# Optimization experiments

Measured on AMD Instinct MI355X. Metric: run time of the kernel, lower is better.

Reference implementation:

```python
import jax, jax.numpy as jnp
import numpy as np

# Static dims (chosen so check_image_size padding is a no-op)
B, C, H, W = 4, 96, 256, 256
NUM_HEADS = 4
WIN_PARAM = 8          # number of windows per dim
SUB = 4                # sub-window pixel size
WIN_H = H // WIN_PARAM  # 32: window pixel size
WIN_W = W // WIN_PARAM
SCALE = (C // NUM_HEADS) ** -0.5


def setup_inputs() -> dict:
    key = jax.random.key(0)
    ks = jax.random.split(key, 4)
    s = 0.02
    return {
        "x": jax.random.normal(ks[0], (B, C, H, W), jnp.float32),
        "q_w": jax.random.normal(ks[1], (C, C), jnp.float32) * s,
        "q_b": jnp.zeros((C,), jnp.float32),
        "kv_w": jax.random.normal(ks[2], (2 * C, C), jnp.float32) * s,
        "kv_b": jnp.zeros((2 * C,), jnp.float32),
        "proj_w": jax.random.normal(ks[3], (C, C), jnp.float32) * s,
        "proj_b": jnp.zeros((C,), jnp.float32),
    }


def reference(x, q_w, q_b, kv_w, kv_b, proj_w, proj_b):
    nWh, nWw = H // WIN_H, W // WIN_W
    nW = nWh * nWw                      # 64 windows
    swh, sww = WIN_H // SUB, WIN_W // SUB
    sNW = swh * sww                     # 64 sub-windows per window
    N = SUB * SUB                       # 16 tokens per sub-window
    d = C // NUM_HEADS

    # B C (nWh wH) (nWw wW) -> B nW wH wW C
    wx = x.reshape(B, C, nWh, WIN_H, nWw, WIN_W).transpose(0, 2, 4, 3, 5, 1)
    wx = wx.reshape(B, nW, WIN_H, WIN_W, C)
    # B nW (swh sub)(sww sub) C -> B nW sNW N C
    sx = wx.reshape(B, nW, swh, SUB, sww, SUB, C).transpose(0, 1, 2, 4, 3, 5, 6)
    sx = sx.reshape(B, nW, sNW, N, C)
    # shuffle: B sNW nW N C
    sh = sx.transpose(0, 2, 1, 3, 4)
    pooled = sh.mean(axis=3)                     # B sNW nW C
    merged = sh.reshape(B, sNW, nW * N, C)       # B sNW (nW N) C

    q = pooled @ q_w.T + q_b                     # B sNW nW C
    kv = merged @ kv_w.T + kv_b                  # B sNW nW*N 2C
    k, v = kv[..., :C], kv[..., C:]

    q = q.reshape(B, sNW, nW, NUM_HEADS, d).transpose(0, 1, 3, 2, 4) * SCALE
    k = k.reshape(B, sNW, nW * N, NUM_HEADS, d).transpose(0, 1, 3, 2, 4)
    v = v.reshape(B, sNW, nW * N, NUM_HEADS, d).transpose(0, 1, 3, 2, 4)

    attn = jax.nn.softmax(jnp.einsum('bshqd,bshkd->bshqk', q, k), axis=-1)
    o = jnp.einsum('bshqk,bshkd->bshqd', attn, v)          # B sNW nH nW d

    # B sNW nH nW d -> B nW sNW (nH d)
    o = o.transpose(0, 3, 1, 2, 4).reshape(B, nW, sNW, C)
    o = o @ proj_w.T + proj_b

    # broadcast each sub-window result to its N tokens (repeat)
    o = jnp.broadcast_to(o[:, :, :, None, :], (B, nW, sNW, N, C))
    # B nW (swh sww)(sub sub) C -> B nW wH wW C
    o = o.reshape(B, nW, swh, sww, SUB, SUB, C).transpose(0, 1, 2, 4, 3, 5, 6)
    o = o.reshape(B, nW, WIN_H, WIN_W, C)
    # B (nWh nWw) wH wW C -> B C H W
    o = o.reshape(B, nWh, nWw, WIN_H, WIN_W, C).transpose(0, 5, 1, 3, 2, 4)
    return o.reshape(B, C, H, W)
```

## Files before the change

### kernel.cpp

```cpp
#include <hip/hip_runtime.h>
#include <hip/hip_bf16.h>
#include <stdint.h>

#define PLANE 65536
#define SCALE_F 0.20412414523193154f
#define PPART 1572864
#define PSTRIDE_F2 786432
#define TI_STRIDE 1572864

typedef __attribute__((ext_vector_type(8))) short short8;
typedef __attribute__((ext_vector_type(4))) float f32x4;

__device__ __forceinline__ unsigned pk2(float a, float b) {
  union { __hip_bfloat162 h; unsigned u; } cv;
  cv.h = __float22bfloat162_rn(make_float2(a, b));
  return cv.u;
}

__global__ __launch_bounds__(256) void prep_kernel(
    const float* __restrict__ kvw, unsigned short* __restrict__ w_a1,
    unsigned short* __restrict__ w_b2) {
  int tid = blockIdx.x * 256 + threadIdx.x;
  int side = tid / 1536;
  int r = tid % 1536;
  int frag = r >> 6;
  int lane = r & 63;
  int tile = frag / 3, ks = frag % 3;
  int od = tile * 16 + (lane & 15);
  int c0 = ks * 32 + (lane >> 4) * 8;
  int h = od >> 5, dd = od & 31;
  unsigned out[4] = {0u, 0u, 0u, 0u};
  if (dd < 24) {
    int row = (side == 0) ? (h * 24 + dd) : (96 + h * 24 + dd);
    const float* src = kvw + row * 96 + c0;
    float4 f0 = *(const float4*)src;
    float4 f1 = *(const float4*)(src + 4);
    out[0] = pk2(f0.x, f0.y); out[1] = pk2(f0.z, f0.w);
    out[2] = pk2(f1.x, f1.y); out[3] = pk2(f1.z, f1.w);
  }
  unsigned* dst =
      (unsigned*)((side == 0) ? w_a1 : w_b2) + (frag * 64 + lane) * 4;
  dst[0] = out[0]; dst[1] = out[1]; dst[2] = out[2]; dst[3] = out[3];
}

__global__ __launch_bounds__(512) void tp_kernel(const float* __restrict__ x,
                                                 unsigned short* __restrict__ xT,
                                                 float2* __restrict__ part2) {
  __shared__ unsigned Lq[48 * 128];
  int blk = blockIdx.x;
  int h = blk & 1;
  int pr = (blk >> 1) & 3;
  int swr = (blk >> 3) & 7;
  int wh = (blk >> 6) & 7;
  int b = blk >> 9;
  int t = threadIdx.x;
  int c4l = t & 31;
  int cpg = t >> 5;
  int ka = c4l >> 3;

  int r = wh * 32 + swr * 4 + pr;
  const float* xrow =
      x + ((size_t)(b * 96) * 256 + r) * 256 + (h * 32 + c4l) * 4;

  float2 pout[3];
  #pragma unroll
  for (int j = 0; j < 3; ++j) {
    int cpair = j * 16 + cpg;
    int cg = cpair >> 2;
    const float* pA = xrow + (size_t)(2 * cpair) * PLANE;
    float4 vA = *(const float4*)pA;
    float4 vB = *(const float4*)(pA + PLANE);
    pout[j].x = (vA.x + vA.y) + (vA.z + vA.w);
    pout[j].y = (vB.x + vB.y) + (vB.z + vB.w);
    unsigned w0 = pk2(vA.x, vB.x), w1 = pk2(vA.y, vB.y);
    unsigned w2 = pk2(vA.z, vB.z), w3 = pk2(vA.w, vB.w);
    int K = ka | ((cg & 7) << 2);
    int base = cpair * 128;
    int c0 = 4 * c4l;
    Lq[base + ((c0 + 0) ^ K)] = w0;
    Lq[base + ((c0 + 1) ^ K)] = w1;
    Lq[base + ((c0 + 2) ^ K)] = w2;
    Lq[base + ((c0 + 3) ^ K)] = w3;
  }

  {
    float2* pp = part2 +
        ((size_t)(((pr * 4 + b) * 8 + swr) * 8 + wh) * 2 + h) * 1536;
    #pragma unroll
    for (int j = 0; j < 3; ++j) pp[j * 512 + t] = pout[j];
  }
  __syncthreads();

  uint4* dst = (uint4*)xT + (size_t)(b * 256 + r) * 3072;
  #pragma unroll
  for (int it = 0; it < 3; ++it) {
    int id = it * 512 + t;
    int sw = id / 192;
    int r1 = id - sw * 192;
    int cg = r1 >> 4;
    int r2 = r1 & 15;
    int pw = r2 >> 2, wwl = r2 & 3;
    int coll = wwl * 32 + sw * 4 + pw;
    int K = wwl | ((cg & 7) << 2);
    int cx = coll ^ K;
    unsigned q0 = Lq[(cg * 4 + 0) * 128 + cx];
    unsigned q1 = Lq[(cg * 4 + 1) * 128 + cx];
    unsigned q2 = Lq[(cg * 4 + 2) * 128 + cx];
    unsigned q3 = Lq[(cg * 4 + 3) * 128 + cx];
    int k32 = pw * 8 + h * 4 + wwl;
    dst[sw * 384 + cg * 32 + k32] = make_uint4(q0, q1, q2, q3);
  }
}

__global__ __launch_bounds__(256) void qgemm_kernel(
    const float2* __restrict__ part2, const float* __restrict__ qw,
    const float* __restrict__ qb, float* __restrict__ q_ws) {
  __shared__ float pl[64 * 97];
  int blk = blockIdx.x;
  int cog = blk & 3, wh = (blk >> 2) & 7, swr = (blk >> 5) & 7, b = blk >> 8;
  int t = threadIdx.x;

  const float2* base = part2 + (size_t)((b * 8 + swr) * 8 + wh) * 3072;
  #pragma unroll
  for (int k = 0; k < 12; ++k) {
    int h = k / 6;
    int r2 = (k % 6) * 256 + t;
    int cpair = r2 >> 5;
    int c4l = t & 31;
    int rest = h * 1536 + r2;
    float2 v0 = base[rest];
    float2 v1 = base[rest + PSTRIDE_F2];
    float2 v2 = base[rest + 2 * PSTRIDE_F2];
    float2 v3 = base[rest + 3 * PSTRIDE_F2];
    float sx = (v0.x + v1.x) + (v2.x + v3.x);
    float sy = (v0.y + v1.y) + (v2.y + v3.y);
    int sw = c4l & 7, ww = h * 4 + (c4l >> 3);
    int row = sw * 8 + ww;
    pl[row * 97 + 2 * cpair] = sx * 0.0625f;
    pl[row * 97 + 2 * cpair + 1] = sy * 0.0625f;
  }
  __syncthreads();

  int wv = t >> 6, lane = t & 63;
  float acc[6] = {0.f, 0.f, 0.f, 0.f, 0.f, 0.f};
  const float* qwr = qw + (cog * 24 + wv) * 96;
  #pragma unroll 4
  for (int c = 0; c < 96; ++c) {
    float v = pl[lane * 97 + c];
    #pragma unroll
    for (int k = 0; k < 6; ++k) acc[k] += v * qwr[k * 384 + c];
  }
  int sw = lane >> 3, ww = lane & 7;
  size_t obase =
      ((size_t)((b * 64 + swr * 8 + sw) * 64) + wh * 8 + ww) * 96;
  #pragma unroll
  for (int k = 0; k < 6; ++k) {
    int co = cog * 24 + k * 4 + wv;
    q_ws[obase + co] = (acc[k] + qb[co]) * SCALE_F;
  }
}

__global__ __launch_bounds__(512, 2) void attn_kernel(
    const unsigned short* __restrict__ xT,
    const unsigned short* __restrict__ w_a1,
    const unsigned short* __restrict__ w_b2, const float* __restrict__ kvb,
    const float* __restrict__ q_ws, float* __restrict__ o_ws) {
  extern __shared__ __align__(16) char sm[];
  char* Ks = sm;
  char* Vs0 = sm + 26624;
  char* Vs1 = sm + 52736;
  char* Ps = sm + 78848;
  float* lbuf = (float*)(sm + 148480);

  int bs = blockIdx.x;
  int b = bs >> 6, s = bs & 63;
  int sh = s >> 3, sw = s & 7;
  int t = threadIdx.x;
  int w = t >> 6, lane = t & 63;
  int l15 = lane & 15, quad = lane >> 4;

  int mhA1 = w >> 2, nhA1 = w & 3;
  int mhA2 = w & 3, nhA2 = w >> 2;
  int head = w & 3, khalf = w >> 2;
  int nh = w >> 2;

  short8 wa[4][3], wb[4][3];
  #pragma unroll
  for (int i = 0; i < 4; ++i)
    #pragma unroll
    for (int k = 0; k < 3; ++k) {
      wa[i][k] = *(const short8*)(w_a1 + (((4 * mhA1 + i) * 3 + k) * 64 + lane) * 8);
      wb[i][k] = *(const short8*)(w_b2 + (((4 * nhA2 + i) * 3 + k) * 64 + lane) * 8);
    }

  short8 qf[4];
  #pragma unroll
  for (int nt = 0; nt < 4; ++nt) {
    short8 f = {0, 0, 0, 0, 0, 0, 0, 0};
    if (quad < 3) {
      const float* qp =
          q_ws + ((size_t)bs * 64 + nt * 16 + l15) * 96 + head * 24 + quad * 8;
      float4 a = *(const float4*)qp;
      float4 c = *(const float4*)(qp + 4);
      union { short8 s8; unsigned u[4]; } cv;
      cv.u[0] = pk2(a.x, a.y); cv.u[1] = pk2(a.z, a.w);
      cv.u[2] = pk2(c.x, c.y); cv.u[3] = pk2(c.z, c.w);
      f = cv.s8;
    }
    qf[nt] = f;
  }

  float bK[4][4];
  #pragma unroll
  for (int i = 0; i < 4; ++i) {
    int od0 = (4 * mhA1 + i) * 16 + quad * 4;
    #pragma unroll
    for (int r = 0; r < 4; ++r) {
      int od = od0 + r, dd = od & 31, h = od >> 5;
      bK[i][r] = (dd < 24) ? kvb[h * 24 + dd] : 0.f;
    }
  }
  float bV[4];
  #pragma unroll
  for (int i = 0; i < 4; ++i) {
    int vd = (4 * nhA2 + i) * 16 + l15, dd = vd & 31, h = vd >> 5;
    bV[i] = (dd < 24) ? kvb[96 + h * 24 + dd] : 0.f;
  }

  f32x4 zz = {0.f, 0.f, 0.f, 0.f};
  f32x4 oacc[2][2];
  #pragma unroll
  for (int m = 0; m < 2; ++m)
    #pragma unroll
    for (int n = 0; n < 2; ++n) oacc[m][n] = zz;
  float lacc[4] = {0.f, 0.f, 0.f, 0.f};

  const char* sb0 = (const char*)xT + (((size_t)(b * 256 + sh * 4) * 8 + sw) * 6144);

  int fo[3][2];
  #pragma unroll
  for (int k = 0; k < 3; ++k)
    #pragma unroll
    for (int hf = 0; hf < 2; ++hf)
      fo[k][hf] = (((k * 4 + quad) * 32) + hf * 16 + l15) * 16;
  int rowA1 = nhA1 * 49152;
  int rowA2 = mhA2 * 49152;

  short8 bxp[2][3], axp[2][3];
  #pragma unroll
  for (int n = 0; n < 2; ++n)
    #pragma unroll
    for (int k = 0; k < 3; ++k)
      bxp[n][k] = *(const short8*)(sb0 + rowA1 + fo[k][n]);
  #pragma unroll
  for (int m = 0; m < 2; ++m)
    #pragma unroll
    for (int k = 0; k < 3; ++k)
      axp[m][k] = *(const short8*)(sb0 + rowA2 + fo[k][m]);

  for (int ti = 0; ti < 8; ++ti) {
    char* Vsb = (ti & 1) ? Vs1 : Vs0;

    {
      f32x4 acc[4][2];
      #pragma unroll
      for (int i = 0; i < 4; ++i)
        #pragma unroll
        for (int n = 0; n < 2; ++n) {
          f32x4 a; a.x = bK[i][0]; a.y = bK[i][1]; a.z = bK[i][2]; a.w = bK[i][3];
          acc[i][n] = a;
        }
      #pragma unroll
      for (int i = 0; i < 4; ++i)
        #pragma unroll
        for (int n = 0; n < 2; ++n)
          #pragma unroll
          for (int k = 0; k < 3; ++k)
            acc[i][n] = __builtin_amdgcn_mfma_f32_16x16x32_bf16(
                wa[i][k], bxp[n][k], acc[i][n], 0, 0, 0);
      #pragma unroll
      for (int i = 0; i < 4; ++i) {
        int od0 = (4 * mhA1 + i) * 16 + quad * 4;
        int dd0 = od0 & 31;
        if (dd0 < 24) {
          int h = od0 >> 5;
          #pragma unroll
          for (int n = 0; n < 2; ++n) {
            int key = (2 * nhA1 + n) * 16 + l15;
            *(int2*)(Ks + key * 208 + (h * 24 + dd0) * 2) =
                make_int2(pk2(acc[i][n].x, acc[i][n].y),
                          pk2(acc[i][n].z, acc[i][n].w));
          }
        }
      }
    }

    {
      #pragma unroll
      for (int m = 0; m < 2; ++m)
        #pragma unroll
        for (int n = 0; n < 4; ++n) {
          f32x4 acc; acc.x = bV[n]; acc.y = bV[n]; acc.z = bV[n]; acc.w = bV[n];
          #pragma unroll
          for (int k = 0; k < 3; ++k)
            acc = __builtin_amdgcn_mfma_f32_16x16x32_bf16(axp[m][k], wb[n][k],
                                                          acc, 0, 0, 0);
          int vd = (4 * nhA2 + n) * 16 + l15;
          int dd = vd & 31, hh = vd >> 5;
          if (dd < 24) {
            int key0 = (2 * mhA2 + m) * 16 + quad * 4;
            *(int2*)(Vsb + (hh * 24 + dd) * 272 + key0 * 2) =
                make_int2(pk2(acc.x, acc.y), pk2(acc.z, acc.w));
          }
        }
    }
    __syncthreads();

    if (ti < 7) {
      const char* sbt = sb0 + (size_t)(ti + 1) * TI_STRIDE;
      #pragma unroll
      for (int n = 0; n < 2; ++n)
        #pragma unroll
        for (int k = 0; k < 3; ++k)
          bxp[n][k] = *(const short8*)(sbt + rowA1 + fo[k][n]);
      #pragma unroll
      for (int m = 0; m < 2; ++m)
        #pragma unroll
        for (int k = 0; k < 3; ++k)
          axp[m][k] = *(const short8*)(sbt + rowA2 + fo[k][m]);
    }

    {
      f32x4 sa[4][4];
      #pragma unroll
      for (int mt = 0; mt < 4; ++mt)
        #pragma unroll
        for (int nt = 0; nt < 4; ++nt) sa[mt][nt] = zz;
      #pragma unroll
      for (int mt = 0; mt < 4; ++mt) {
        int key = khalf * 64 + mt * 16 + l15;
        short8 ak = {0, 0, 0, 0, 0, 0, 0, 0};
        if (quad < 3)
          ak = *(const short8*)(Ks + key * 208 + head * 48 + quad * 16);
        #pragma unroll
        for (int nt = 0; nt < 4; ++nt)
          sa[mt][nt] = __builtin_amdgcn_mfma_f32_16x16x32_bf16(ak, qf[nt],
                                                               sa[mt][nt], 0, 0, 0);
      }
      #pragma unroll
      for (int mt = 0; mt < 4; ++mt) {
        int key0 = khalf * 64 + mt * 16 + quad * 4;
        #pragma unroll
        for (int nt = 0; nt < 4; ++nt) {
          float e0 = __expf(sa[mt][nt].x), e1 = __expf(sa[mt][nt].y);
          float e2 = __expf(sa[mt][nt].z), e3 = __expf(sa[mt][nt].w);
          lacc[nt] += (e0 + e1) + (e2 + e3);
          *(int2*)(Ps + head * 17408 + (nt * 16 + l15) * 272 + key0 * 2) =
              make_int2(pk2(e0, e1), pk2(e2, e3));
        }
      }
      if (ti == 7) {
        #pragma unroll
        for (int nt = 0; nt < 4; ++nt) {
          float v = lacc[nt];
          v += __shfl_xor(v, 16);
          v += __shfl_xor(v, 32);
          if (quad == 0) lbuf[(head * 2 + khalf) * 64 + nt * 16 + l15] = v;
        }
      }
    }
    __syncthreads();

    #pragma unroll
    for (int ks = 0; ks < 4; ++ks) {
      short8 av[2];
      #pragma unroll
      for (int mt = 0; mt < 2; ++mt) {
        int dloc = mt * 16 + l15;
        int prow = head * 24 + (dloc < 24 ? dloc : 0);
        av[mt] = *(const short8*)(Vsb + prow * 272 + ks * 64 + quad * 16);
      }
      #pragma unroll
      for (int n = 0; n < 2; ++n) {
        short8 bp = *(const short8*)(Ps + head * 17408 +
                                     ((2 * nh + n) * 16 + l15) * 272 +
                                     ks * 64 + quad * 16);
        #pragma unroll
        for (int mt = 0; mt < 2; ++mt)
          oacc[mt][n] = __builtin_amdgcn_mfma_f32_16x16x32_bf16(av[mt], bp,
                                                                oacc[mt][n], 0, 0, 0);
      }
    }
  }

  #pragma unroll
  for (int n = 0; n < 2; ++n) {
    int q = (2 * nh + n) * 16 + l15;
    float l = lbuf[(head * 2 + 0) * 64 + q] + lbuf[(head * 2 + 1) * 64 + q];
    float inv = 1.0f / l;
    #pragma unroll
    for (int mt = 0; mt < 2; ++mt)
      #pragma unroll
      for (int r = 0; r < 4; ++r) {
        int d = mt * 16 + quad * 4 + r;
        if (d < 24)
          o_ws[((size_t)bs * 64 + q) * 96 + head * 24 + d] = oacc[mt][n][r] * inv;
      }
  }
}

__global__ __launch_bounds__(256) void proj_kernel(const float* __restrict__ o_ws,
                                                   const float* __restrict__ pw,
                                                   const float* __restrict__ pb,
                                                   float* __restrict__ out) {
  __shared__ float ol[64 * 97];
  int blk = blockIdx.x;
  int cog = blk & 3, sh = (blk >> 2) & 7, wh = (blk >> 5) & 7, b = blk >> 8;
  int t = threadIdx.x;

  #pragma unroll
  for (int k = 0; k < 24; ++k) {
    int id = k * 256 + t;
    int pair = id / 96, c = id - pair * 96;
    int sw = pair >> 3, ww = pair & 7;
    ol[pair * 97 + c] =
        o_ws[(((size_t)(b * 64 + sh * 8 + sw)) * 64 + wh * 8 + ww) * 96 + c];
  }
  __syncthreads();

  int wv = t >> 6, lane = t & 63;
  int pair = (lane & 7) * 8 + (lane >> 3);
  float acc[6] = {0.f, 0.f, 0.f, 0.f, 0.f, 0.f};
  const float* pwr = pw + (cog * 24 + wv) * 96;
  #pragma unroll 4
  for (int c = 0; c < 96; ++c) {
    float v = ol[pair * 97 + c];
    #pragma unroll
    for (int k = 0; k < 6; ++k) acc[k] += v * pwr[k * 384 + c];
  }

  #pragma unroll
  for (int k = 0; k < 6; ++k) {
    int co = cog * 24 + k * 4 + wv;
    float val = acc[k] + pb[co];
    float4 pk = make_float4(val, val, val, val);
    size_t rowbase = ((size_t)(b * 96 + co) * 256 + wh * 32 + sh * 4) * 256;
    #pragma unroll
    for (int ph = 0; ph < 4; ++ph)
      *(float4*)(out + rowbase + ph * 256 + lane * 4) = pk;
  }
}

extern "C" void kernel_launch(void* const* d_in, const int* in_sizes, int n_in,
                              void* d_out, int out_size, void* d_ws,
                              size_t ws_size, hipStream_t stream) {
  const float* x = (const float*)d_in[0];
  const float* qw = (const float*)d_in[1];
  const float* qb = (const float*)d_in[2];
  const float* kvw = (const float*)d_in[3];
  const float* kvb = (const float*)d_in[4];
  const float* pw = (const float*)d_in[5];
  const float* pb = (const float*)d_in[6];

  float* pooled_part = (float*)d_ws;
  float* q_ws = pooled_part + 4 * PPART;
  float* o_ws = q_ws + PPART;
  unsigned short* w_a1 = (unsigned short*)(o_ws + PPART);
  unsigned short* w_b2 = w_a1 + 12288;
  unsigned short* xT = w_b2 + 12288;

  static int attn_lds = 150528;
  (void)hipFuncSetAttribute((const void*)attn_kernel,
                            hipFuncAttributeMaxDynamicSharedMemorySize,
                            attn_lds);

  hipLaunchKernelGGL(prep_kernel, dim3(12), dim3(256), 0, stream, kvw, w_a1, w_b2);
  hipLaunchKernelGGL(tp_kernel, dim3(2048), dim3(512), 0, stream, x, xT,
                     (float2*)pooled_part);
  hipLaunchKernelGGL(qgemm_kernel, dim3(1024), dim3(256), 0, stream,
                     (const float2*)pooled_part, qw, qb, q_ws);
  hipLaunchKernelGGL(attn_kernel, dim3(256), dim3(512), attn_lds, stream, xT,
                     w_a1, w_b2, kvb, q_ws, o_ws);
  hipLaunchKernelGGL(proj_kernel, dim3(1024), dim3(256), 0, stream, o_ws, pw, pb,
                     (float*)d_out);
}
```

Baseline: 320.3 us.

## Swizzle V/P LDS tiles, dedupe x fragment loads, move prefetch later

```diff
diff --git a/kernel.cpp b/kernel.cpp
--- a/kernel.cpp
+++ b/kernel.cpp
@@ -168,9 +168,9 @@
   extern __shared__ __align__(16) char sm[];
   char* Ks = sm;
   char* Vs0 = sm + 26624;
-  char* Vs1 = sm + 52736;
-  char* Ps = sm + 78848;
-  float* lbuf = (float*)(sm + 148480);
+  char* Vs1 = sm + 51200;
+  char* Ps = sm + 75776;
+  float* lbuf = (float*)(sm + 141312);
 
   int bs = blockIdx.x;
   int b = bs >> 6, s = bs & 63;
@@ -243,20 +243,14 @@
     #pragma unroll
     for (int hf = 0; hf < 2; ++hf)
       fo[k][hf] = (((k * 4 + quad) * 32) + hf * 16 + l15) * 16;
-  int rowA1 = nhA1 * 49152;
-  int rowA2 = mhA2 * 49152;
-
-  short8 bxp[2][3], axp[2][3];
+  int rowF = (w & 3) * 49152;
+
+  short8 fx[2][3];
   #pragma unroll
   for (int n = 0; n < 2; ++n)
     #pragma unroll
     for (int k = 0; k < 3; ++k)
-      bxp[n][k] = *(const short8*)(sb0 + rowA1 + fo[k][n]);
-  #pragma unroll
-  for (int m = 0; m < 2; ++m)
-    #pragma unroll
-    for (int k = 0; k < 3; ++k)
-      axp[m][k] = *(const short8*)(sb0 + rowA2 + fo[k][m]);
+      fx[n][k] = *(const short8*)(sb0 + rowF + fo[k][n]);
 
   for (int ti = 0; ti < 8; ++ti) {
     char* Vsb = (ti & 1) ? Vs1 : Vs0;
@@ -277,7 +271,7 @@
           #pragma unroll
           for (int k = 0; k < 3; ++k)
             acc[i][n] = __builtin_amdgcn_mfma_f32_16x16x32_bf16(
-                wa[i][k], bxp[n][k], acc[i][n], 0, 0, 0);
+                wa[i][k], fx[n][k], acc[i][n], 0, 0, 0);
       #pragma unroll
       for (int i = 0; i < 4; ++i) {
         int od0 = (4 * mhA1 + i) * 16 + quad * 4;
@@ -303,32 +297,19 @@
           f32x4 acc; acc.x = bV[n]; acc.y = bV[n]; acc.z = bV[n]; acc.w = bV[n];
           #pragma unroll
           for (int k = 0; k < 3; ++k)
-            acc = __builtin_amdgcn_mfma_f32_16x16x32_bf16(axp[m][k], wb[n][k],
+            acc = __builtin_amdgcn_mfma_f32_16x16x32_bf16(fx[m][k], wb[n][k],
                                                           acc, 0, 0, 0);
           int vd = (4 * nhA2 + n) * 16 + l15;
           int dd = vd & 31, hh = vd >> 5;
           if (dd < 24) {
-            int key0 = (2 * mhA2 + m) * 16 + quad * 4;
-            *(int2*)(Vsb + (hh * 24 + dd) * 272 + key0 * 2) =
+            int rowv = hh * 24 + dd;
+            int colb = ((2 * mhA2 + m) * 16 + quad * 4) * 2;
+            *(int2*)(Vsb + rowv * 256 + (colb ^ ((rowv & 7) << 4))) =
                 make_int2(pk2(acc.x, acc.y), pk2(acc.z, acc.w));
           }
         }
     }
     __syncthreads();
-
-    if (ti < 7) {
-      const char* sbt = sb0 + (size_t)(ti + 1) * TI_STRIDE;
-      #pragma unroll
-      for (int n = 0; n < 2; ++n)
-        #pragma unroll
-        for (int k = 0; k < 3; ++k)
-          bxp[n][k] = *(const short8*)(sbt + rowA1 + fo[k][n]);
-      #pragma unroll
-      for (int m = 0; m < 2; ++m)
-        #pragma unroll
-        for (int k = 0; k < 3; ++k)
-          axp[m][k] = *(const short8*)(sbt + rowA2 + fo[k][m]);
-    }
 
     {
       f32x4 sa[4][4];
@@ -349,13 +330,14 @@
       }
       #pragma unroll
       for (int mt = 0; mt < 4; ++mt) {
-        int key0 = khalf * 64 + mt * 16 + quad * 4;
+        int colb = (khalf * 64 + mt * 16 + quad * 4) * 2;
         #pragma unroll
         for (int nt = 0; nt < 4; ++nt) {
           float e0 = __expf(sa[mt][nt].x), e1 = __expf(sa[mt][nt].y);
           float e2 = __expf(sa[mt][nt].z), e3 = __expf(sa[mt][nt].w);
           lacc[nt] += (e0 + e1) + (e2 + e3);
-          *(int2*)(Ps + head * 17408 + (nt * 16 + l15) * 272 + key0 * 2) =
+          int row = nt * 16 + l15;
+          *(int2*)(Ps + head * 16384 + row * 256 + (colb ^ ((row & 7) << 4))) =
               make_int2(pk2(e0, e1), pk2(e2, e3));
         }
       }
@@ -371,20 +353,30 @@
     }
     __syncthreads();
 
+    if (ti < 7) {
+      const char* sbt = sb0 + (size_t)(ti + 1) * TI_STRIDE;
+      #pragma unroll
+      for (int n = 0; n < 2; ++n)
+        #pragma unroll
+        for (int k = 0; k < 3; ++k)
+          fx[n][k] = *(const short8*)(sbt + rowF + fo[k][n]);
+    }
+
     #pragma unroll
     for (int ks = 0; ks < 4; ++ks) {
+      int colb = ks * 64 + quad * 16;
       short8 av[2];
       #pragma unroll
       for (int mt = 0; mt < 2; ++mt) {
         int dloc = mt * 16 + l15;
         int prow = head * 24 + (dloc < 24 ? dloc : 0);
-        av[mt] = *(const short8*)(Vsb + prow * 272 + ks * 64 + quad * 16);
+        av[mt] = *(const short8*)(Vsb + prow * 256 + (colb ^ ((prow & 7) << 4)));
       }
       #pragma unroll
       for (int n = 0; n < 2; ++n) {
-        short8 bp = *(const short8*)(Ps + head * 17408 +
-                                     ((2 * nh + n) * 16 + l15) * 272 +
-                                     ks * 64 + quad * 16);
+        int row = (2 * nh + n) * 16 + l15;
+        short8 bp = *(const short8*)(Ps + head * 16384 + row * 256 +
+                                     (colb ^ ((row & 7) << 4)));
         #pragma unroll
         for (int mt = 0; mt < 2; ++mt)
           oacc[mt][n] = __builtin_amdgcn_mfma_f32_16x16x32_bf16(av[mt], bp,
@@ -469,7 +461,7 @@
   unsigned short* w_b2 = w_a1 + 12288;
   unsigned short* xT = w_b2 + 12288;
 
-  static int attn_lds = 150528;
+  static int attn_lds = 143360;
   (void)hipFuncSetAttribute((const void*)attn_kernel,
                             hipFuncAttributeMaxDynamicSharedMemorySize,
                             attn_lds);
```

New measurement: 337.1 us. +5.2%, slower.
